# Kernel optimization log

Hardware: AMD Instinct MI355X
Metric: run time of the kernel (lower is better)

## Reference

```python
import jax, jax.numpy as jnp
import numpy as np

N = 100000   # nodes
E = 1600000  # edges
F = 128      # in_feats
H = 4        # heads
D = 32       # out_feats per head
NEG_SLOPE = 0.2


def setup_inputs() -> dict:
    key = jax.random.key(0)
    k1, k2, k3, k4, k5, k6 = jax.random.split(key, 6)
    feat = jax.random.normal(k1, (N, F), dtype=jnp.float32)
    W = jax.random.normal(k2, (H * D, F), dtype=jnp.float32) * (1.0 / np.sqrt(F))
    attn_l = jax.random.normal(k3, (1, H, D), dtype=jnp.float32) * 0.1
    attn_r = jax.random.normal(k4, (1, H, D), dtype=jnp.float32) * 0.1
    src = jax.random.randint(k5, (E,), 0, N, dtype=jnp.int32)
    dst = jax.random.randint(k6, (E,), 0, N, dtype=jnp.int32)
    return {"feat": feat, "W": W, "attn_l": attn_l, "attn_r": attn_r, "src": src, "dst": dst}


def reference(feat, W, attn_l, attn_r, src, dst):
    # fc projection: [N, F] -> [N, H, D]
    h = (feat @ W.T).reshape(N, H, D)
    # per-node attention logits [N, H]
    el = jnp.sum(h * attn_l, axis=-1)
    er = jnp.sum(h * attn_r, axis=-1)
    # edge scores: el[src] + er[dst] -> leaky relu  [E, H]
    e = jax.nn.leaky_relu(el[src] + er[dst], negative_slope=NEG_SLOPE)
    # segment softmax over edges grouped by destination node, per head
    m = jax.ops.segment_max(e, dst, num_segments=N)          # [N, H]
    ex = jnp.exp(e - m[dst])                                 # [E, H]
    s = jax.ops.segment_sum(ex, dst, num_segments=N)         # [N, H]
    alpha = ex / s[dst]                                      # [E, H]
    # weighted sparse aggregation: out[dst] += alpha * h[src]
    msgs = alpha[:, :, None] * h[src]                        # [E, H, D]
    rst = jax.ops.segment_sum(msgs, dst, num_segments=N)     # [N, H, D]
    return rst
```

## Files before the change

kernel.cpp:

```cpp
#include <hip/hip_runtime.h>

constexpr int N_NODES = 100000;
constexpr int E_EDGES = 1600000;
constexpr int NBLK    = (N_NODES + 1023) / 1024;
constexpr int NBLOCKS = (N_NODES + 63) / 64;

typedef _Float16 f16;
typedef _Float16 f16x2 __attribute__((ext_vector_type(2)));
typedef _Float16 f16x4 __attribute__((ext_vector_type(4)));
typedef _Float16 f16x8 __attribute__((ext_vector_type(8)));
typedef float f32x4 __attribute__((ext_vector_type(4)));

__global__ __launch_bounds__(256) void k_gemm_hist(
        const float* __restrict__ feat, const float* __restrict__ W,
        const float* __restrict__ attn_l, const float* __restrict__ attn_r,
        f16* __restrict__ h2, float* __restrict__ el, float* __restrict__ er,
        const int4* __restrict__ dst4, int* __restrict__ deg,
        int4* __restrict__ rank4) {
    __shared__ f16 Wlds[128 * 128];
    char* wb = (char*)Wlds;
    const int tid = threadIdx.x;
    const int bid = blockIdx.x;

    const int te = bid * 256 + tid;
    const bool he = te < E_EDGES / 4;
    int4 dd = he ? dst4[te] : make_int4(0, 0, 0, 0);

    {
        int n = tid >> 1;
        int kh = (tid & 1) * 64;
        const float* wsrc = W + n * 128 + kh;
#pragma unroll
        for (int q = 0; q < 8; ++q) {
            float4 u0 = *reinterpret_cast<const float4*>(wsrc + q * 8);
            float4 u1 = *reinterpret_cast<const float4*>(wsrc + q * 8 + 4);
            f16x8 v;
            v[0] = (f16)u0.x; v[1] = (f16)u0.y; v[2] = (f16)u0.z; v[3] = (f16)u0.w;
            v[4] = (f16)u1.x; v[5] = (f16)u1.y; v[6] = (f16)u1.z; v[7] = (f16)u1.w;
            unsigned byte = (unsigned)(n * 256 + kh * 2 + q * 16) ^ ((n & 7) << 4);
            *reinterpret_cast<f16x8*>(wb + byte) = v;
        }
    }
    __syncthreads();

    const int wav  = tid >> 6;
    const int lane = tid & 63;
    const int la = lane & 15;
    const int lb = lane >> 4;
    const int row0w = bid * 64 + wav * 16;

    int rowA = row0w + la;
    if (rowA >= N_NODES) rowA = N_NODES - 1;
    const float* ap = feat + (size_t)rowA * 128 + lb * 8;
    float4 u[8];
#pragma unroll
    for (int kk = 0; kk < 4; ++kk) {
        u[kk * 2 + 0] = *reinterpret_cast<const float4*>(ap + kk * 32);
        u[kk * 2 + 1] = *reinterpret_cast<const float4*>(ap + kk * 32 + 4);
    }

    int r0 = 0, r1 = 0, r2 = 0, r3 = 0;
    if (he) {
        r0 = atomicAdd(&deg[dd.x], 1);
        r1 = atomicAdd(&deg[dd.y], 1);
        r2 = atomicAdd(&deg[dd.z], 1);
        r3 = atomicAdd(&deg[dd.w], 1);
    }

    f16x8 ffrag[4];
#pragma unroll
    for (int kk = 0; kk < 4; ++kk) {
        float4 u0 = u[kk * 2 + 0];
        float4 u1 = u[kk * 2 + 1];
        f16x8 a;
        a[0] = (f16)u0.x; a[1] = (f16)u0.y; a[2] = (f16)u0.z; a[3] = (f16)u0.w;
        a[4] = (f16)u1.x; a[5] = (f16)u1.y; a[6] = (f16)u1.z; a[7] = (f16)u1.w;
        ffrag[kk] = a;
    }

    f32x4 acc[8];
#pragma unroll
    for (int t = 0; t < 8; ++t) acc[t] = (f32x4){0.f, 0.f, 0.f, 0.f};

#pragma unroll
    for (int t = 0; t < 8; ++t) {
        int wrow = t * 16 + la;
#pragma unroll
        for (int kk = 0; kk < 4; ++kk) {
            unsigned byte = (unsigned)(wrow * 256 + (kk * 32 + lb * 8) * 2) ^ ((wrow & 7) << 4);
            f16x8 b = *reinterpret_cast<const f16x8*>(wb + byte);
            acc[t] = __builtin_amdgcn_mfma_f32_16x16x32_f16(b, ffrag[kk], acc[t], 0, 0, 0);
        }
    }

    const int row = row0w + la;
    const bool ok = row < N_NODES;
    if (ok) {
#pragma unroll
        for (int t = 0; t < 8; ++t) {
            f16x4 hv;
            hv.x = (f16)acc[t][0]; hv.y = (f16)acc[t][1];
            hv.z = (f16)acc[t][2]; hv.w = (f16)acc[t][3];
            *reinterpret_cast<f16x4*>(&h2[(size_t)row * 128 + t * 16 + lb * 4]) = hv;
        }
    }

    float sl[4] = {0.f, 0.f, 0.f, 0.f}, sr[4] = {0.f, 0.f, 0.f, 0.f};
#pragma unroll
    for (int t = 0; t < 8; ++t) {
        float4 alv = reinterpret_cast<const float4*>(attn_l)[t * 4 + lb];
        float4 arv = reinterpret_cast<const float4*>(attn_r)[t * 4 + lb];
        int g = t >> 1;
        sl[g] += acc[t][0] * alv.x + acc[t][1] * alv.y + acc[t][2] * alv.z + acc[t][3] * alv.w;
        sr[g] += acc[t][0] * arv.x + acc[t][1] * arv.y + acc[t][2] * arv.z + acc[t][3] * arv.w;
    }
#pragma unroll
    for (int g = 0; g < 4; ++g) {
        sl[g] += __shfl_xor(sl[g], 16, 64);
        sl[g] += __shfl_xor(sl[g], 32, 64);
        sr[g] += __shfl_xor(sr[g], 16, 64);
        sr[g] += __shfl_xor(sr[g], 32, 64);
    }
    if (lb == 0 && ok) {
        *reinterpret_cast<float4*>(el + (size_t)row * 4) = make_float4(sl[0], sl[1], sl[2], sl[3]);
        *reinterpret_cast<float4*>(er + (size_t)row * 4) = make_float4(sr[0], sr[1], sr[2], sr[3]);
    }

    if (he) rank4[te] = make_int4(r0, r1, r2, r3);
}

__global__ void k_bsum(const int* __restrict__ deg, int* __restrict__ aux) {
    int tid = threadIdx.x;
    int i0 = blockIdx.x * 1024 + tid * 4;
    int sum = 0;
#pragma unroll
    for (int j = 0; j < 4; ++j)
        if (i0 + j < N_NODES) sum += (deg[i0 + j] + 3) & ~3;
#pragma unroll
    for (int m = 32; m; m >>= 1) sum += __shfl_xor(sum, m, 64);
    __shared__ int wsums[4];
    if ((tid & 63) == 0) wsums[tid >> 6] = sum;
    __syncthreads();
    if (tid == 0) aux[blockIdx.x] = wsums[0] + wsums[1] + wsums[2] + wsums[3];
}

__global__ void k_bscan(const int* __restrict__ deg, const int* __restrict__ aux,
                        int* __restrict__ start, int* __restrict__ ssrc,
                        f16* __restrict__ h2, float* __restrict__ el) {
    if (blockIdx.x == 0 && threadIdx.x == 0) {
        float4 z = make_float4(0.f, 0.f, 0.f, 0.f);
        float4* hrow = reinterpret_cast<float4*>(h2 + (size_t)N_NODES * 128);
#pragma unroll
        for (int q = 0; q < 16; ++q) hrow[q] = z;
        *reinterpret_cast<float4*>(el + (size_t)N_NODES * 4) =
            make_float4(-1e4f, -1e4f, -1e4f, -1e4f);
    }
    int tid = threadIdx.x;
    int lane = tid & 63;
    int wid = tid >> 6;

    __shared__ int sbase;
    if (tid < 64) {
        int a = 0;
        if (tid < blockIdx.x) a += aux[tid];
        if (tid + 64 < blockIdx.x) a += aux[tid + 64];
#pragma unroll
        for (int m = 32; m; m >>= 1) a += __shfl_xor(a, m, 64);
        if (tid == 0) sbase = a;
    }

    int i0 = blockIdx.x * 1024 + tid * 4;
    int v[4], pv[4];
#pragma unroll
    for (int j = 0; j < 4; ++j) {
        v[j]  = (i0 + j < N_NODES) ? deg[i0 + j] : 0;
        pv[j] = (v[j] + 3) & ~3;
    }
    int tsum = pv[0] + pv[1] + pv[2] + pv[3];
    int x = tsum;
#pragma unroll
    for (int d = 1; d < 64; d <<= 1) {
        int t = __shfl_up(x, d, 64);
        if (lane >= d) x += t;
    }
    __shared__ int wsums[4];
    if (lane == 63) wsums[wid] = x;
    __syncthreads();
    int base = sbase;
#pragma unroll
    for (int w = 0; w < 4; ++w)
        if (w < wid) base += wsums[w];
    int p = base + x - tsum;
#pragma unroll
    for (int j = 0; j < 4; ++j) {
        if (i0 + j < N_NODES) {
            start[i0 + j] = p;
            for (int q = v[j]; q < pv[j]; ++q) ssrc[p + q] = N_NODES;
        }
        p += pv[j];
    }
}

__global__ void k_scatter(const int4* __restrict__ src4, const int4* __restrict__ dst4,
                          const int4* __restrict__ rank4, const int* __restrict__ start,
                          int* __restrict__ ssrc) {
    int t = blockIdx.x * blockDim.x + threadIdx.x;
    if (t >= E_EDGES / 4) return;
    int4 s = src4[t];
    int4 d = dst4[t];
    int4 r = rank4[t];
    int p0 = start[d.x] + r.x;
    int p1 = start[d.y] + r.y;
    int p2 = start[d.z] + r.z;
    int p3 = start[d.w] + r.w;
    ssrc[p0] = s.x;
    ssrc[p1] = s.y;
    ssrc[p2] = s.z;
    ssrc[p3] = s.w;
}

__global__ __launch_bounds__(128) void k_aggr(const f16* __restrict__ h2,
                                              const float* __restrict__ el,
                                              const float* __restrict__ er,
                                              const int* __restrict__ ssrc,
                                              const int* __restrict__ start,
                                              const int* __restrict__ deg,
                                              float* __restrict__ out) {
    int n = blockIdx.x * 2 + (threadIdx.x >> 6);
    if (n >= N_NODES) return;
    int lane = threadIdx.x & 63;
    int half = lane >> 5;
    int l5 = lane & 31;
    int g = l5 >> 3;
    int d = deg[n];
    int nit = ((d + 3) & ~3) >> 2;
    int s4 = __builtin_amdgcn_readfirstlane(start[n] >> 2);
    const int4* ssrc4 = reinterpret_cast<const int4*>(ssrc);
    float ern = er[n * 4 + g];

    f16x4 acA = {0, 0, 0, 0}, acB = {0, 0, 0, 0};
    float swA = 0.f, swB = 0.f;

    if (nit > 0) {
        int4 sv = ssrc4[s4];
        for (int it = 0; it < nit; ++it) {
            int4 svn = ssrc4[s4 + it + 1];

            int nA = half ? sv.y : sv.x;
            int nB = half ? sv.w : sv.z;
            float eA = el[(size_t)nA * 4 + g];
            float eB = el[(size_t)nB * 4 + g];
            f16x4 qA = *reinterpret_cast<const f16x4*>(h2 + (size_t)nA * 128 + l5 * 4);
            f16x4 qB = *reinterpret_cast<const f16x4*>(h2 + (size_t)nB * 128 + l5 * 4);

            float xA = eA + ern; xA = fmaxf(xA, 0.2f * xA);
            float xB = eB + ern; xB = fmaxf(xB, 0.2f * xB);
            float wA = __expf(xA);
            float wB = __expf(xB);

            f16 hA = (f16)wA; f16x4 wvA = {hA, hA, hA, hA};
            f16 hB = (f16)wB; f16x4 wvB = {hB, hB, hB, hB};
            acA += wvA * qA; swA += wA;
            acB += wvB * qB; swB += wB;

            sv = svn;
        }
    }

    f16x4 ac = acA + acB;
    float swv = swA + swB;
    union { f16x4 v; int u[2]; } uu; uu.v = ac;
    int o0 = __shfl_xor(uu.u[0], 32, 64);
    int o1 = __shfl_xor(uu.u[1], 32, 64);
    union { int u[2]; f16x4 v; } vv; vv.u[0] = o0; vv.u[1] = o1;
    ac += vv.v;
    swv += __shfl_xor(swv, 32, 64);

    float inv = (d > 0) ? 1.0f / swv : 0.0f;
    if (half == 0) {
        float4 o = make_float4((float)ac[0] * inv, (float)ac[1] * inv,
                               (float)ac[2] * inv, (float)ac[3] * inv);
        *reinterpret_cast<float4*>(out + (size_t)n * 128 + l5 * 4) = o;
    }
}

extern "C" void kernel_launch(void* const* d_in, const int* in_sizes, int n_in,
                              void* d_out, int out_size, void* d_ws, size_t ws_size,
                              hipStream_t stream) {
    const float* feat   = (const float*)d_in[0];
    const float* W      = (const float*)d_in[1];
    const float* attn_l = (const float*)d_in[2];
    const float* attn_r = (const float*)d_in[3];
    const int*   src    = (const int*)d_in[4];
    const int*   dst    = (const int*)d_in[5];
    float* out = (float*)d_out;

    f16*   h2    = (f16*)d_ws;
    float* el    = (float*)(h2 + (size_t)(N_NODES + 8) * 128);
    float* er    = el + (size_t)(N_NODES + 4) * 4;
    int*   deg   = (int*)(er + (size_t)N_NODES * 4);
    int*   start = deg + N_NODES;
    int*   rank  = start + N_NODES;
    int*   ssrc  = rank + E_EDGES;
    int*   aux   = ssrc + E_EDGES + 3 * N_NODES + 64;

    hipMemsetAsync(deg, 0, N_NODES * sizeof(int), stream);

    k_gemm_hist<<<NBLOCKS, 256, 0, stream>>>(feat, W, attn_l, attn_r, h2, el, er,
                                             (const int4*)dst, deg, (int4*)rank);
    k_bsum<<<NBLK, 256, 0, stream>>>(deg, aux);
    k_bscan<<<NBLK, 256, 0, stream>>>(deg, aux, start, ssrc, h2, el);
    k_scatter<<<(E_EDGES / 4 + 255) / 256, 256, 0, stream>>>(
        (const int4*)src, (const int4*)dst, (const int4*)rank, start, ssrc);
    k_aggr<<<(N_NODES + 1) / 2, 128, 0, stream>>>(h2, el, er, ssrc, start, deg, out);
}
```

Measured before the change: 191.2 us.

## Replicate degree histogram across eight copies to spread atomic contention

The degree-counting atomics in the GEMM kernel now target one of eight replicated histograms, chosen by block index. The bsum kernel reduces the replicas into the final degree array, and the scan writes a start offset for each replica so the scatter can compute slots consistently. The aim is to spread atomic traffic over more addresses and cut same-address contention on hot nodes. In exchange it adds a larger memset, eight times the reads in the reduction and scan, and a larger start table that the scatter gathers from.

```diff
diff --git a/kernel.cpp b/kernel.cpp
--- a/kernel.cpp
+++ b/kernel.cpp
@@ -4,6 +4,7 @@
 constexpr int E_EDGES = 1600000;
 constexpr int NBLK    = (N_NODES + 1023) / 1024;
 constexpr int NBLOCKS = (N_NODES + 63) / 64;
+constexpr int NREP    = 8;
 
 typedef _Float16 f16;
 typedef _Float16 f16x2 __attribute__((ext_vector_type(2)));
@@ -15,7 +16,7 @@
         const float* __restrict__ feat, const float* __restrict__ W,
         const float* __restrict__ attn_l, const float* __restrict__ attn_r,
         f16* __restrict__ h2, float* __restrict__ el, float* __restrict__ er,
-        const int4* __restrict__ dst4, int* __restrict__ deg,
+        const int4* __restrict__ dst4, int* __restrict__ deg_r,
         int4* __restrict__ rank4) {
     __shared__ f16 Wlds[128 * 128];
     char* wb = (char*)Wlds;
@@ -25,6 +26,7 @@
     const int te = bid * 256 + tid;
     const bool he = te < E_EDGES / 4;
     int4 dd = he ? dst4[te] : make_int4(0, 0, 0, 0);
+    int* degrep = deg_r + (size_t)(bid & (NREP - 1)) * N_NODES;
 
     {
         int n = tid >> 1;
@@ -61,10 +63,10 @@
 
     int r0 = 0, r1 = 0, r2 = 0, r3 = 0;
     if (he) {
-        r0 = atomicAdd(&deg[dd.x], 1);
-        r1 = atomicAdd(&deg[dd.y], 1);
-        r2 = atomicAdd(&deg[dd.z], 1);
-        r3 = atomicAdd(&deg[dd.w], 1);
+        r0 = atomicAdd(&degrep[dd.x], 1);
+        r1 = atomicAdd(&degrep[dd.y], 1);
+        r2 = atomicAdd(&degrep[dd.z], 1);
+        r3 = atomicAdd(&degrep[dd.w], 1);
     }
 
     f16x8 ffrag[4];
@@ -129,13 +131,21 @@
     if (he) rank4[te] = make_int4(r0, r1, r2, r3);
 }
 
-__global__ void k_bsum(const int* __restrict__ deg, int* __restrict__ aux) {
+__global__ void k_bsum(const int* __restrict__ deg_r, int* __restrict__ deg,
+                       int* __restrict__ aux) {
     int tid = threadIdx.x;
     int i0 = blockIdx.x * 1024 + tid * 4;
     int sum = 0;
 #pragma unroll
-    for (int j = 0; j < 4; ++j)
-        if (i0 + j < N_NODES) sum += (deg[i0 + j] + 3) & ~3;
+    for (int j = 0; j < 4; ++j) {
+        if (i0 + j < N_NODES) {
+            int d = 0;
+#pragma unroll
+            for (int r = 0; r < NREP; ++r) d += deg_r[(size_t)r * N_NODES + i0 + j];
+            deg[i0 + j] = d;
+            sum += (d + 3) & ~3;
+        }
+    }
 #pragma unroll
     for (int m = 32; m; m >>= 1) sum += __shfl_xor(sum, m, 64);
     __shared__ int wsums[4];
@@ -144,8 +154,10 @@
     if (tid == 0) aux[blockIdx.x] = wsums[0] + wsums[1] + wsums[2] + wsums[3];
 }
 
-__global__ void k_bscan(const int* __restrict__ deg, const int* __restrict__ aux,
-                        int* __restrict__ start, int* __restrict__ ssrc,
+__global__ void k_bscan(const int* __restrict__ deg, const int* __restrict__ deg_r,
+                        const int* __restrict__ aux,
+                        int* __restrict__ start, int* __restrict__ start_r,
+                        int* __restrict__ ssrc,
                         f16* __restrict__ h2, float* __restrict__ el) {
     if (blockIdx.x == 0 && threadIdx.x == 0) {
         float4 z = make_float4(0.f, 0.f, 0.f, 0.f);
@@ -194,7 +206,14 @@
 #pragma unroll
     for (int j = 0; j < 4; ++j) {
         if (i0 + j < N_NODES) {
-            start[i0 + j] = p;
+            int n = i0 + j;
+            start[n] = p;
+            int running = p;
+#pragma unroll
+            for (int r = 0; r < NREP; ++r) {
+                start_r[(size_t)r * N_NODES + n] = running;
+                running += deg_r[(size_t)r * N_NODES + n];
+            }
             for (int q = v[j]; q < pv[j]; ++q) ssrc[p + q] = N_NODES;
         }
         p += pv[j];
@@ -202,17 +221,18 @@
 }
 
 __global__ void k_scatter(const int4* __restrict__ src4, const int4* __restrict__ dst4,
-                          const int4* __restrict__ rank4, const int* __restrict__ start,
+                          const int4* __restrict__ rank4, const int* __restrict__ start_r,
                           int* __restrict__ ssrc) {
     int t = blockIdx.x * blockDim.x + threadIdx.x;
     if (t >= E_EDGES / 4) return;
+    const int* sr = start_r + (size_t)((t >> 8) & (NREP - 1)) * N_NODES;
     int4 s = src4[t];
     int4 d = dst4[t];
     int4 r = rank4[t];
-    int p0 = start[d.x] + r.x;
-    int p1 = start[d.y] + r.y;
-    int p2 = start[d.z] + r.z;
-    int p3 = start[d.w] + r.w;
+    int p0 = sr[d.x] + r.x;
+    int p1 = sr[d.y] + r.y;
+    int p2 = sr[d.z] + r.z;
+    int p3 = sr[d.w] + r.w;
     ssrc[p0] = s.x;
     ssrc[p1] = s.y;
     ssrc[p2] = s.z;
@@ -295,22 +315,24 @@
     const int*   dst    = (const int*)d_in[5];
     float* out = (float*)d_out;
 
-    f16*   h2    = (f16*)d_ws;
-    float* el    = (float*)(h2 + (size_t)(N_NODES + 8) * 128);
-    float* er    = el + (size_t)(N_NODES + 4) * 4;
-    int*   deg   = (int*)(er + (size_t)N_NODES * 4);
-    int*   start = deg + N_NODES;
-    int*   rank  = start + N_NODES;
-    int*   ssrc  = rank + E_EDGES;
-    int*   aux   = ssrc + E_EDGES + 3 * N_NODES + 64;
-
-    hipMemsetAsync(deg, 0, N_NODES * sizeof(int), stream);
+    f16*   h2      = (f16*)d_ws;
+    float* el      = (float*)(h2 + (size_t)(N_NODES + 8) * 128);
+    float* er      = el + (size_t)(N_NODES + 4) * 4;
+    int*   deg     = (int*)(er + (size_t)N_NODES * 4);
+    int*   start   = deg + N_NODES;
+    int*   rank    = start + N_NODES;
+    int*   ssrc    = rank + E_EDGES;
+    int*   deg_r   = ssrc + E_EDGES + 3 * N_NODES + 64;
+    int*   start_r = deg_r + NREP * N_NODES;
+    int*   aux     = start_r + NREP * N_NODES;
+
+    hipMemsetAsync(deg_r, 0, (size_t)NREP * N_NODES * sizeof(int), stream);
 
     k_gemm_hist<<<NBLOCKS, 256, 0, stream>>>(feat, W, attn_l, attn_r, h2, el, er,
-                                             (const int4*)dst, deg, (int4*)rank);
-    k_bsum<<<NBLK, 256, 0, stream>>>(deg, aux);
-    k_bscan<<<NBLK, 256, 0, stream>>>(deg, aux, start, ssrc, h2, el);
+                                             (const int4*)dst, deg_r, (int4*)rank);
+    k_bsum<<<NBLK, 256, 0, stream>>>(deg_r, deg, aux);
+    k_bscan<<<NBLK, 256, 0, stream>>>(deg, deg_r, aux, start, start_r, ssrc, h2, el);
     k_scatter<<<(E_EDGES / 4 + 255) / 256, 256, 0, stream>>>(
-        (const int4*)src, (const int4*)dst, (const int4*)rank, start, ssrc);
+        (const int4*)src, (const int4*)dst, (const int4*)rank, start_r, ssrc);
     k_aggr<<<(N_NODES + 1) / 2, 128, 0, stream>>>(h2, el, er, ssrc, start, deg, out);
 }
```

After: 194.2 us. Within noise of the previous version (+1.5%).
